# Performance work log

Hardware: AMD Instinct MI355X
Metric: run time of the kernel (lower is better)

Reference implementation:

```python
import jax, jax.numpy as jnp
import numpy as np

B, SEQ, D, H, PRED = 131072, 150, 2, 64, 150


def setup_inputs() -> dict:
    key = jax.random.key(0)
    ks = jax.random.split(key, 5)
    s1 = 1.0 / np.sqrt(D)  # torch Linear default init bounds
    s2 = 1.0 / np.sqrt(H)
    return {
        "x": jax.random.normal(ks[0], (B, SEQ, D), jnp.float32),
        "W1": jax.random.uniform(ks[1], (D, H), jnp.float32, -s1, s1),
        "b1": jax.random.uniform(ks[2], (H,), jnp.float32, -s1, s1),
        "W2": jax.random.uniform(ks[3], (H, D), jnp.float32, -s2, s2),
        "b2": jax.random.uniform(ks[4], (D,), jnp.float32, -s2, s2),
    }


def reference(x, W1, b1, W2, b2):
    # ODE RHS: autonomous 2-layer MLP, f(t, y) = tanh(y W1 + b1) W2 + b2
    def f(y):
        return jnp.tanh(y @ W1 + b1) @ W2 + b2

    y0 = x[:, -1, :]  # [B, D]
    t = jnp.linspace(0.0, float(PRED), PRED)  # 150 grid points -> 149 steps
    dts = t[1:] - t[:-1]  # each = 150/149

    # torchdiffeq method='rk4' uses the 3/8-rule fixed-grid step (rk4_alt_step_func)
    def step(y, dt):
        k1 = f(y)
        k2 = f(y + dt * k1 / 3.0)
        k3 = f(y + dt * (k2 - k1 / 3.0))
        k4 = f(y + dt * (k1 - k2 + k3))
        y1 = y + dt * (k1 + 3.0 * (k2 + k3) + k4) / 8.0
        return y1, y1

    _, ys = jax.lax.scan(step, y0, dts)  # ys: [PRED-1, B, D]
    pred = jnp.concatenate([y0[None], ys], axis=0)  # [PRED, B, D]
    return pred.transpose(1, 0, 2)  # [B, PRED, D]
```

## Files before the change

### kernel.cpp

```cpp
#include <hip/hip_runtime.h>

#ifndef __has_builtin
#define __has_builtin(x) 0
#endif

__device__ __forceinline__ float fast_exp2(float x) {
#if __has_builtin(__builtin_amdgcn_exp2f)
  return __builtin_amdgcn_exp2f(x);
#else
  return exp2f(x);
#endif
}
__device__ __forceinline__ float fast_rcp(float x) {
#if __has_builtin(__builtin_amdgcn_rcpf)
  return __builtin_amdgcn_rcpf(x);
#else
  return 1.0f / x;
#endif
}

namespace {
constexpr int kB = 131072;
constexpr int kSeq = 150;
constexpr int kD = 2;
constexpr int kH = 64;
constexpr int kPred = 150;
constexpr int kSteps = kPred - 1;
constexpr float kDt = 150.0f / 149.0f;
constexpr float kC = 2.8853900817779268f;
}

__device__ __forceinline__ void feval(float y0, float y1,
                                      const float4* __restrict__ sw,
                                      const float4* __restrict__ sb4,
                                      float base0, float base1,
                                      float& f0, float& f1) {
  float a0 = 0.0f, a1 = 0.0f, c0 = 0.0f, c1 = 0.0f;
#pragma unroll 4
  for (int q = 0; q < kH / 4; ++q) {
    float4 bb = sb4[q];
    float4 w0 = sw[4 * q + 0];
    float p0 = fmaf(y0, w0.x, fmaf(y1, w0.y, bb.x));
    float r0 = fast_rcp(1.0f + fast_exp2(p0));
    a0 = fmaf(r0, w0.z, a0);
    a1 = fmaf(r0, w0.w, a1);
    float4 w1 = sw[4 * q + 1];
    float p1 = fmaf(y0, w1.x, fmaf(y1, w1.y, bb.y));
    float r1 = fast_rcp(1.0f + fast_exp2(p1));
    c0 = fmaf(r1, w1.z, c0);
    c1 = fmaf(r1, w1.w, c1);
    float4 w2 = sw[4 * q + 2];
    float p2 = fmaf(y0, w2.x, fmaf(y1, w2.y, bb.z));
    float r2 = fast_rcp(1.0f + fast_exp2(p2));
    a0 = fmaf(r2, w2.z, a0);
    a1 = fmaf(r2, w2.w, a1);
    float4 w3 = sw[4 * q + 3];
    float p3 = fmaf(y0, w3.x, fmaf(y1, w3.y, bb.w));
    float r3 = fast_rcp(1.0f + fast_exp2(p3));
    c0 = fmaf(r3, w3.z, c0);
    c1 = fmaf(r3, w3.w, c1);
  }
  f0 = base0 + a0 + c0;
  f1 = base1 + a1 + c1;
}

__global__ __launch_bounds__(256, 2) void ode_kernel(
    const float* __restrict__ x, const float* __restrict__ W1,
    const float* __restrict__ b1, const float* __restrict__ W2,
    const float* __restrict__ b2, float* __restrict__ out) {
  __shared__ float4 sw[kH];
  __shared__ float4 sb4[kH / 4];
  __shared__ float sbase[2];

  const int t = threadIdx.x;
  if (t < kH) {
    sw[t] = make_float4(W1[t] * kC, W1[kH + t] * kC,
                        -2.0f * W2[2 * t], -2.0f * W2[2 * t + 1]);
    reinterpret_cast<float*>(sb4)[t] = b1[t] * kC;
  }
  if (t < 2) {
    float s = b2[t];
    for (int j = 0; j < kH; ++j) s += W2[2 * j + t];
    sbase[t] = s;
  }
  __syncthreads();
  const float base0 = sbase[0], base1 = sbase[1];

  const long bidx = (long)blockIdx.x * blockDim.x + t;
  const float* xp = x + bidx * (long)(kSeq * kD) + (kSeq - 1) * kD;
  float y0 = xp[0];
  float y1 = xp[1];
  float* op = out + bidx * (long)(kPred * kD);

  float py0 = y0, py1 = y1;
  constexpr float DT = kDt, DT3 = kDt / 3.0f, DT8 = kDt / 8.0f;

  for (int s = 1; s <= kSteps; ++s) {
    float k1x, k1y, k2x, k2y, k3x, k3y, k4x, k4y;
    feval(y0, y1, sw, sb4, base0, base1, k1x, k1y);
    feval(fmaf(DT3, k1x, y0), fmaf(DT3, k1y, y1), sw, sb4, base0, base1, k2x, k2y);
    feval(fmaf(DT, k2x, fmaf(-DT3, k1x, y0)),
          fmaf(DT, k2y, fmaf(-DT3, k1y, y1)), sw, sb4, base0, base1, k3x, k3y);
    feval(fmaf(DT, k1x - k2x + k3x, y0),
          fmaf(DT, k1y - k2y + k3y, y1), sw, sb4, base0, base1, k4x, k4y);
    y0 = fmaf(DT8, k1x + 3.0f * (k2x + k3x) + k4x, y0);
    y1 = fmaf(DT8, k1y + 3.0f * (k2y + k3y) + k4y, y1);

    if (s & 1) {
      float4 v = make_float4(py0, py1, y0, y1);
      *reinterpret_cast<float4*>(op + (long)(s - 1) * 2) = v;
    } else {
      py0 = y0;
      py1 = y1;
    }
  }
}

extern "C" void kernel_launch(void* const* d_in, const int* in_sizes, int n_in,
                              void* d_out, int out_size, void* d_ws,
                              size_t ws_size, hipStream_t stream) {
  const float* x = (const float*)d_in[0];
  const float* W1 = (const float*)d_in[1];
  const float* b1 = (const float*)d_in[2];
  const float* W2 = (const float*)d_in[3];
  const float* b2 = (const float*)d_in[4];
  float* out = (float*)d_out;

  dim3 grid(kB / 256);
  dim3 block(256);
  hipLaunchKernelGGL(ode_kernel, grid, block, 0, stream, x, W1, b1, W2, b2,
                     out);
}
```

Baseline: 1.433 ms.

## Split hidden units across four lanes with register weights and DPP reduction

Each batch element is now handled by four adjacent lanes, each owning 16 of the 64 hidden units. Each lane keeps its weights in registers instead of reading them from shared memory. Partial MLP outputs are combined with two DPP cross-lane adds, and the b2 bias term is split across the four lanes. This gives four times as many threads to raise occupancy and hide the latency of the serial RK4 chain, and it removes LDS weight loads. The cost is extra DPP reduction steps in every function evaluation, duplicated y-update arithmetic across the four lanes, and stores issued by only one lane in four.

```diff
diff --git a/kernel.cpp b/kernel.cpp
--- a/kernel.cpp
+++ b/kernel.cpp
@@ -28,87 +28,93 @@
 constexpr int kSteps = kPred - 1;
 constexpr float kDt = 150.0f / 149.0f;
 constexpr float kC = 2.8853900817779268f;
+constexpr int kSplit = 4;
+constexpr int kHper = kH / kSplit;
+constexpr int kBlock = 256;
+constexpr int kElemsPerBlock = kBlock / kSplit;
 }
 
-__device__ __forceinline__ void feval(float y0, float y1,
-                                      const float4* __restrict__ sw,
-                                      const float4* __restrict__ sb4,
-                                      float base0, float base1,
-                                      float& f0, float& f1) {
-  float a0 = 0.0f, a1 = 0.0f, c0 = 0.0f, c1 = 0.0f;
-#pragma unroll 4
-  for (int q = 0; q < kH / 4; ++q) {
-    float4 bb = sb4[q];
-    float4 w0 = sw[4 * q + 0];
-    float p0 = fmaf(y0, w0.x, fmaf(y1, w0.y, bb.x));
-    float r0 = fast_rcp(1.0f + fast_exp2(p0));
-    a0 = fmaf(r0, w0.z, a0);
-    a1 = fmaf(r0, w0.w, a1);
-    float4 w1 = sw[4 * q + 1];
-    float p1 = fmaf(y0, w1.x, fmaf(y1, w1.y, bb.y));
-    float r1 = fast_rcp(1.0f + fast_exp2(p1));
-    c0 = fmaf(r1, w1.z, c0);
-    c1 = fmaf(r1, w1.w, c1);
-    float4 w2 = sw[4 * q + 2];
-    float p2 = fmaf(y0, w2.x, fmaf(y1, w2.y, bb.z));
-    float r2 = fast_rcp(1.0f + fast_exp2(p2));
-    a0 = fmaf(r2, w2.z, a0);
-    a1 = fmaf(r2, w2.w, a1);
-    float4 w3 = sw[4 * q + 3];
-    float p3 = fmaf(y0, w3.x, fmaf(y1, w3.y, bb.w));
-    float r3 = fast_rcp(1.0f + fast_exp2(p3));
-    c0 = fmaf(r3, w3.z, c0);
-    c1 = fmaf(r3, w3.w, c1);
-  }
-  f0 = base0 + a0 + c0;
-  f1 = base1 + a1 + c1;
+__device__ __forceinline__ float dpp_xor1_add(float v) {
+  int s = __builtin_amdgcn_update_dpp(0, __float_as_int(v), 0xB1, 0xF, 0xF, true);
+  return v + __int_as_float(s);
+}
+__device__ __forceinline__ float dpp_xor2_add(float v) {
+  int s = __builtin_amdgcn_update_dpp(0, __float_as_int(v), 0x4E, 0xF, 0xF, true);
+  return v + __int_as_float(s);
 }
 
-__global__ __launch_bounds__(256, 2) void ode_kernel(
+__global__ __launch_bounds__(kBlock, 4) void ode_kernel(
     const float* __restrict__ x, const float* __restrict__ W1,
     const float* __restrict__ b1, const float* __restrict__ W2,
     const float* __restrict__ b2, float* __restrict__ out) {
-  __shared__ float4 sw[kH];
-  __shared__ float4 sb4[kH / 4];
-  __shared__ float sbase[2];
+  const int t = threadIdx.x;
+  const int part = t & (kSplit - 1);
+  const int j0 = part * kHper;
 
-  const int t = threadIdx.x;
-  if (t < kH) {
-    sw[t] = make_float4(W1[t] * kC, W1[kH + t] * kC,
-                        -2.0f * W2[2 * t], -2.0f * W2[2 * t + 1]);
-    reinterpret_cast<float*>(sb4)[t] = b1[t] * kC;
+  float wx[kHper], wy[kHper], wz[kHper], ww[kHper], wb[kHper];
+#pragma unroll
+  for (int i = 0; i < kHper; ++i) {
+    const int j = j0 + i;
+    wx[i] = W1[j] * kC;
+    wy[i] = W1[kH + j] * kC;
+    wb[i] = b1[j] * kC;
+    wz[i] = -2.0f * W2[2 * j];
+    ww[i] = -2.0f * W2[2 * j + 1];
   }
-  if (t < 2) {
-    float s = b2[t];
-    for (int j = 0; j < kH; ++j) s += W2[2 * j + t];
-    sbase[t] = s;
+  float pb0 = 0.25f * b2[0];
+  float pb1 = 0.25f * b2[1];
+#pragma unroll
+  for (int i = 0; i < kHper; ++i) {
+    pb0 = fmaf(-0.5f, wz[i], pb0);
+    pb1 = fmaf(-0.5f, ww[i], pb1);
   }
-  __syncthreads();
-  const float base0 = sbase[0], base1 = sbase[1];
 
-  const long bidx = (long)blockIdx.x * blockDim.x + t;
-  const float* xp = x + bidx * (long)(kSeq * kD) + (kSeq - 1) * kD;
+  const long elem = (long)blockIdx.x * kElemsPerBlock + (t >> 2);
+  const float* xp = x + elem * (long)(kSeq * kD) + (kSeq - 1) * kD;
   float y0 = xp[0];
   float y1 = xp[1];
-  float* op = out + bidx * (long)(kPred * kD);
+  float* op = out + elem * (long)(kPred * kD);
+
+  auto feval = [&](float u0, float u1, float& f0, float& f1) {
+    float a0 = pb0, a1 = pb1, c0 = 0.0f, c1 = 0.0f;
+#pragma unroll
+    for (int i = 0; i < kHper; i += 2) {
+      float p0 = fmaf(u0, wx[i], fmaf(u1, wy[i], wb[i]));
+      float r0 = fast_rcp(1.0f + fast_exp2(p0));
+      a0 = fmaf(r0, wz[i], a0);
+      a1 = fmaf(r0, ww[i], a1);
+      float p1 = fmaf(u0, wx[i + 1], fmaf(u1, wy[i + 1], wb[i + 1]));
+      float r1 = fast_rcp(1.0f + fast_exp2(p1));
+      c0 = fmaf(r1, wz[i + 1], c0);
+      c1 = fmaf(r1, ww[i + 1], c1);
+    }
+    a0 += c0;
+    a1 += c1;
+    a0 = dpp_xor2_add(dpp_xor1_add(a0));
+    a1 = dpp_xor2_add(dpp_xor1_add(a1));
+    f0 = a0;
+    f1 = a1;
+  };
 
   float py0 = y0, py1 = y1;
   constexpr float DT = kDt, DT3 = kDt / 3.0f, DT8 = kDt / 8.0f;
 
   for (int s = 1; s <= kSteps; ++s) {
     float k1x, k1y, k2x, k2y, k3x, k3y, k4x, k4y;
-    feval(y0, y1, sw, sb4, base0, base1, k1x, k1y);
-    feval(fmaf(DT3, k1x, y0), fmaf(DT3, k1y, y1), sw, sb4, base0, base1, k2x, k2y);
+    feval(y0, y1, k1x, k1y);
+    feval(fmaf(DT3, k1x, y0), fmaf(DT3, k1y, y1), k2x, k2y);
     feval(fmaf(DT, k2x, fmaf(-DT3, k1x, y0)),
-          fmaf(DT, k2y, fmaf(-DT3, k1y, y1)), sw, sb4, base0, base1, k3x, k3y);
+          fmaf(DT, k2y, fmaf(-DT3, k1y, y1)), k3x, k3y);
     feval(fmaf(DT, k1x - k2x + k3x, y0),
-          fmaf(DT, k1y - k2y + k3y, y1), sw, sb4, base0, base1, k4x, k4y);
+          fmaf(DT, k1y - k2y + k3y, y1), k4x, k4y);
     y0 = fmaf(DT8, k1x + 3.0f * (k2x + k3x) + k4x, y0);
     y1 = fmaf(DT8, k1y + 3.0f * (k2y + k3y) + k4y, y1);
 
     if (s & 1) {
-      float4 v = make_float4(py0, py1, y0, y1);
-      *reinterpret_cast<float4*>(op + (long)(s - 1) * 2) = v;
+      if (part == 0) {
+        float4 v = make_float4(py0, py1, y0, y1);
+        *reinterpret_cast<float4*>(op + (long)(s - 1) * 2) = v;
+      }
     } else {
       py0 = y0;
       py1 = y1;
@@ -126,8 +132,8 @@
   const float* b2 = (const float*)d_in[4];
   float* out = (float*)d_out;
 
-  dim3 grid(kB / 256);
-  dim3 block(256);
+  dim3 grid(kB * kSplit / kBlock);
+  dim3 block(kBlock);
   hipLaunchKernelGGL(ode_kernel, grid, block, 0, stream, x, W1, b1, W2, b2,
                      out);
 }
```

Result: faster. 1.350 ms (-5.8%).
